# Optimization experiments

Measured on AMD Instinct MI355X. Metric: run time of the kernel, lower is better.

The kernel has to match this reference:

```python
import jax, jax.numpy as jnp
import numpy as np

B, IN, H, F, T = 4096, 1024, 1024, 128, 3
LN_EPS = 1e-5


def setup_inputs() -> dict:
    key = jax.random.key(0)
    ks = jax.random.split(key, 12)
    inp = {
        "input_": jax.random.normal(ks[0], (B, IN), jnp.float32),
        "hx": jax.random.normal(ks[1], (B, H), jnp.float32),
        "cx": jax.random.normal(ks[2], (B, H), jnp.float32),
        "topic_w": jax.random.uniform(ks[3], (B, T), jnp.float32),
        # factorized gate weights (init scales per reset_parameters)
        "w_ih_a": jax.random.normal(ks[4], (4 * H, F), jnp.float32) / jnp.sqrt(F),
        "w_ih_b": jnp.full((F, T), 0.1 / T, jnp.float32),
        "w_ih_c": jax.random.normal(ks[5], (F, IN), jnp.float32) / jnp.sqrt(IN),
        "w_hh_a": 0.1 * jax.random.normal(ks[6], (4 * H, F), jnp.float32),
        "w_hh_b": jnp.full((F, T), 0.1 / T, jnp.float32),
        "w_hh_c": 0.1 * jax.random.normal(ks[7], (F, H), jnp.float32),
        # theta transforms: weight=0, bias=1 per reset_parameters
        "th_ih_w": jnp.zeros((T, T), jnp.float32),
        "th_ih_b": jnp.ones((T,), jnp.float32),
        "th_hh_w": jnp.zeros((T, T), jnp.float32),
        "th_hh_b": jnp.ones((T,), jnp.float32),
        # layernorm params
        "ln_i_w": jnp.ones((4 * H,), jnp.float32),
        "ln_i_b": jnp.zeros((4 * H,), jnp.float32),
        "ln_h_w": jnp.ones((4 * H,), jnp.float32),
        "ln_h_b": jnp.zeros((4 * H,), jnp.float32),
        "ln_c_w": jnp.ones((H,), jnp.float32),
        "ln_c_b": jnp.zeros((H,), jnp.float32),
    }
    return inp


def _ln(x, w, b):
    mu = x.mean(-1, keepdims=True)
    var = ((x - mu) ** 2).mean(-1, keepdims=True)
    return (x - mu) * jax.lax.rsqrt(var + LN_EPS) * w + b


def reference(input_, hx, cx, topic_w,
              w_ih_a, w_ih_b, w_ih_c, w_hh_a, w_hh_b, w_hh_c,
              th_ih_w, th_ih_b, th_hh_w, th_hh_b,
              ln_i_w, ln_i_b, ln_h_w, ln_h_b, ln_c_w, ln_c_b):
    # factorized input gates: ((x @ C^T) * (theta(topic) @ B^T)) @ A^T
    scale_i = (topic_w @ th_ih_w.T + th_ih_b) @ w_ih_b.T            # [B, F]
    igates = ((input_ @ w_ih_c.T) * scale_i) @ w_ih_a.T             # [B, 4H]
    scale_h = (topic_w @ th_hh_w.T + th_hh_b) @ w_hh_b.T            # [B, F]
    hgates = ((hx @ w_hh_c.T) * scale_h) @ w_hh_a.T                 # [B, 4H]

    gates = _ln(igates, ln_i_w, ln_i_b) + _ln(hgates, ln_h_w, ln_h_b)
    i, f, g, o = jnp.split(gates, 4, axis=1)
    i = jax.nn.sigmoid(i)
    f = jax.nn.sigmoid(f)
    g = jnp.tanh(g)  # dropout p=0 -> identity
    o = jax.nn.sigmoid(o)
    cy = _ln(f * cx + i * g, ln_c_w, ln_c_b)
    hy = o * jnp.tanh(cy)
    return hy, cy
```

## Files before the change

kernel.cpp:

```cpp
#include <hip/hip_runtime.h>

typedef unsigned short ushort_t;
typedef __attribute__((ext_vector_type(8))) short bf8_t;
typedef __attribute__((ext_vector_type(4))) float f4_t;

#define B_   4096
#define IN_  1024
#define H_   1024
#define F_   128
#define G4_  4096
#define EPS_ 1e-5f

#define NG1   512
#define NPREP 256
#define NGRAM 128

__device__ __forceinline__ float us2f(unsigned short s) {
  union { unsigned int u; float f; } v;
  v.u = ((unsigned int)s) << 16;
  return v.f;
}
__device__ __forceinline__ unsigned short f2us(float f) {
  union { float f; unsigned int u; } v;
  v.f = f;
  unsigned int r = (v.u + 0x7fffu + ((v.u >> 16) & 1u)) >> 16;
  return (unsigned short)r;
}
__device__ __forceinline__ float sigf(float x) { return 1.0f / (1.0f + __expf(-x)); }
__device__ __forceinline__ float tanh_f(float x) { return 1.0f - 2.0f / (1.0f + __expf(2.0f * x)); }

__device__ __forceinline__ int detect_fp32(const void* disc) {
  return ((const unsigned int*)disc)[0] == 0x3F800000u;
}
__device__ __forceinline__ float ldf(const void* p, int i, int fp32) {
  return fp32 ? ((const float*)p)[i] : us2f(((const ushort_t*)p)[i]);
}
__device__ __forceinline__ void ld8(const void* p, int idx, float* o, int fp32) {
  if (fp32) {
    const float4* q = (const float4*)((const float*)p + idx);
    float4 v0 = q[0], v1 = q[1];
    o[0]=v0.x; o[1]=v0.y; o[2]=v0.z; o[3]=v0.w;
    o[4]=v1.x; o[5]=v1.y; o[6]=v1.z; o[7]=v1.w;
  } else {
    uint4 v = *(const uint4*)((const ushort_t*)p + idx);
    const ushort_t* pv = (const ushort_t*)&v;
    #pragma unroll
    for (int i = 0; i < 8; i++) o[i] = us2f(pv[i]);
  }
}
__device__ __forceinline__ bf8_t cvt8p(const float* f) {
  union { bf8_t v; unsigned int u[4]; } r;
  const unsigned int* ui = (const unsigned int*)f;
  #pragma unroll
  for (int i = 0; i < 4; i++) {
    unsigned int lo = ui[2 * i] + 0x8000u;
    unsigned int hi = ui[2 * i + 1] + 0x8000u;
    r.u[i] = __builtin_amdgcn_perm(hi, lo, 0x07060302u);
  }
  return r.v;
}

__global__ __launch_bounds__(256, 4) void k_stageA(
    const void* __restrict__ X0, const void* __restrict__ X1,
    const void* __restrict__ Wc0, const void* __restrict__ Wc1,
    const void* __restrict__ topic,
    const void* __restrict__ thw0, const void* __restrict__ thw1,
    const void* __restrict__ thb0, const void* __restrict__ thb1,
    const void* __restrict__ wsb0, const void* __restrict__ wsb1,
    const void* __restrict__ Ai, const void* __restrict__ Ah,
    const void* __restrict__ lnwi, const void* __restrict__ lnwh,
    ushort_t* __restrict__ wb,
    float* __restrict__ cm_i, float* __restrict__ cm_h,
    float* __restrict__ g_i, float* __restrict__ g_h,
    float* __restrict__ C0, float* __restrict__ C1)
{
  __shared__ __align__(16) char lds_raw[32768];
  int bid = blockIdx.x, tid = threadIdx.x;
  int fp32 = detect_fp32(lnwi);

  if (bid < NG1) {
    int rb = bid >> 1, mat = bid & 1;
    const void* X   = mat ? X1 : X0;
    const void* W   = mat ? Wc1 : Wc0;
    const void* thw = mat ? thw1 : thw0;
    const void* thb = mat ? thb1 : thb0;
    const void* wbp = mat ? wsb1 : wsb0;
    float* C = mat ? C1 : C0;
    int lane = tid & 63, w = tid >> 6;
    int quad = lane >> 4, lcol = lane & 15;
    int brow0 = rb * 16;

    #pragma unroll
    for (int p = 0; p < 8; p++) {
      int fl = p * 2048 + tid * 8;
      int r = fl >> 10, cidx = fl & 1023;
      float t8[8];
      ld8(X, (brow0 + r) * IN_ + cidx, t8, fp32);
      bf8_t v = cvt8p(t8);
      int byte = (r * 2048 + cidx * 2) ^ ((r & 7) << 4);
      *(bf8_t*)(lds_raw + byte) = v;
    }
    __syncthreads();

    f4_t acc[2];
    acc[0] = (f4_t){0.f, 0.f, 0.f, 0.f};
    acc[1] = (f4_t){0.f, 0.f, 0.f, 0.f};

    int wrow = w * 32 + lcol;
    int quad8 = quad * 8;
    int afbase = lcol * 2048 + quad * 16;
    int afxor = (lcol & 7) << 4;

#define AF_(kc) (*(const bf8_t*)(lds_raw + ((afbase + (kc) * 64) ^ afxor)))
#define LOADW_(buf, kc) { \
      ld8(W, (wrow)      * IN_ + (kc) * 32 + quad8, buf[0], fp32); \
      ld8(W, (wrow + 16) * IN_ + (kc) * 32 + quad8, buf[1], fp32); }
#define STEPK_(buf, kc) { \
      bf8_t af_ = AF_(kc); \
      acc[0] = __builtin_amdgcn_mfma_f32_16x16x32_bf16(af_, cvt8p(buf[0]), acc[0], 0, 0, 0); \
      acc[1] = __builtin_amdgcn_mfma_f32_16x16x32_bf16(af_, cvt8p(buf[1]), acc[1], 0, 0, 0); }

    float pb0[2][8], pb1[2][8];
    LOADW_(pb0, 0);
    LOADW_(pb1, 1);
    #pragma unroll
    for (int kc = 0; kc < 32; kc += 2) {
      STEPK_(pb0, kc);
      if (kc + 2 < 32) LOADW_(pb0, kc + 2);
      STEPK_(pb1, kc + 1);
      if (kc + 3 < 32) LOADW_(pb1, kc + 3);
    }
#undef AF_
#undef LOADW_
#undef STEPK_

    float thwf[3][3], thbf[3];
    #pragma unroll
    for (int t = 0; t < 3; t++) {
      thbf[t] = ldf(thb, t, fp32);
      #pragma unroll
      for (int t2 = 0; t2 < 3; t2++) thwf[t][t2] = ldf(thw, t * 3 + t2, fp32);
    }
    float tmpv[4][3];
    #pragma unroll
    for (int reg = 0; reg < 4; reg++) {
      int b = brow0 + quad * 4 + reg;
      float tp0 = ldf(topic, b * 3 + 0, fp32);
      float tp1 = ldf(topic, b * 3 + 1, fp32);
      float tp2 = ldf(topic, b * 3 + 2, fp32);
      #pragma unroll
      for (int t = 0; t < 3; t++)
        tmpv[reg][t] = thbf[t] + tp0 * thwf[t][0] + tp1 * thwf[t][1] + tp2 * thwf[t][2];
    }
    #pragma unroll
    for (int t = 0; t < 2; t++) {
      int f = (w * 2 + t) * 16 + lcol;
      float wv0 = ldf(wbp, f * 3 + 0, fp32);
      float wv1 = ldf(wbp, f * 3 + 1, fp32);
      float wv2 = ldf(wbp, f * 3 + 2, fp32);
      #pragma unroll
      for (int reg = 0; reg < 4; reg++) {
        float sc = tmpv[reg][0] * wv0 + tmpv[reg][1] * wv1 + tmpv[reg][2] * wv2;
        C[(brow0 + quad * 4 + reg) * F_ + f] = acc[t][reg] * sc;
      }
    }
  } else if (bid < NG1 + NPREP) {
    int t = bid - NG1;
    #pragma unroll
    for (int i = 0; i < 16; i++) {
      int e = i * 256 + tid;
      int c = e >> 9, l = (e >> 3) & 63, j = e & 7;
      int k = c * 32 + ((l >> 4) << 3) + j;
      int n = t * 16 + (l & 15);
      float v;
      if (k < 128) v = ldf(Ai, n * F_ + k, fp32) * ldf(lnwi, n, fp32);
      else         v = ldf(Ah, n * F_ + (k - 128), fp32) * ldf(lnwh, n, fp32);
      wb[(size_t)t * 4096 + e] = f2us(v);
    }
    const void* A = (tid < 128) ? Ai : Ah;
    float* cm = (tid < 128) ? cm_i : cm_h;
    int f = tid & 127;
    float s = 0.f;
    #pragma unroll
    for (int i = 0; i < 16; i++) s += ldf(A, (t * 16 + i) * F_ + f, fp32);
    atomicAdd(&cm[f], s);
  } else {
    int g = bid - (NG1 + NPREP);
    int fblk = g & 3, mat = (g >> 2) & 1, z = g >> 3;
    const void* A = mat ? Ah : Ai;
    float* G = mat ? g_h : g_i;
    float (*As)[128] = (float(*)[128])lds_raw;
    int f1_0 = fblk * 32;
    int tf2 = tid & 31, tf1 = tid >> 5;
    float acc[4][4] = {};
    int nbase = z * 256;
    for (int n0 = nbase; n0 < nbase + 256; n0 += 32) {
      #pragma unroll
      for (int j = 0; j < 2; j++) {
        int idx = tid + 256 * j;
        int nn = idx >> 4, f8 = (idx & 15) * 8;
        float t[8];
        ld8(A, (n0 + nn) * F_ + f8, t, fp32);
        #pragma unroll
        for (int i = 0; i < 8; i++) As[nn][f8 + i] = t[i];
      }
      __syncthreads();
      #pragma unroll 4
      for (int nn = 0; nn < 32; nn++) {
        float4 a1 = *(const float4*)&As[nn][f1_0 + 4 * tf1];
        float4 a2 = *(const float4*)&As[nn][4 * tf2];
        const float* x1 = (const float*)&a1;
        const float* x2 = (const float*)&a2;
        #pragma unroll
        for (int i = 0; i < 4; i++)
          #pragma unroll
          for (int j = 0; j < 4; j++) acc[i][j] += x1[i] * x2[j];
      }
      __syncthreads();
    }
    #pragma unroll
    for (int i = 0; i < 4; i++)
      #pragma unroll
      for (int j = 0; j < 4; j++)
        atomicAdd(&G[(f1_0 + 4 * tf1 + i) * F_ + 4 * tf2 + j], acc[i][j]);
  }
}

__global__ __launch_bounds__(256, 4) void k_stats2(
    const float* __restrict__ C0, const float* __restrict__ C1,
    const float* __restrict__ g_i, const float* __restrict__ g_h,
    const float* __restrict__ cm_i, const float* __restrict__ cm_h,
    float* __restrict__ mrs_i, float* __restrict__ mrs_h,
    ushort_t* __restrict__ xb)
{
  int bid = blockIdx.x;
  int rb = bid >> 1, mat = bid & 1;
  const float* C  = mat ? C1 : C0;
  const float* G  = mat ? g_h : g_i;
  const float* cm = mat ? cm_h : cm_i;
  float* mrs = mat ? mrs_h : mrs_i;
  int kbase = mat ? 128 : 0;

  int tid = threadIdx.x;
  int lane = tid & 63, w = tid >> 6;
  int quad = lane >> 4, lcol = lane & 15;
  int b0 = rb * 16;

  __shared__ float p1part[4][16];
  __shared__ float p2s[16];
  __shared__ float rs_s[16];

  bf8_t af[4];
  float p2p = 0.f;
  #pragma unroll
  for (int kc = 0; kc < 4; kc++) {
    int kb = kc * 32 + quad * 8;
    const float4* q = (const float4*)(C + (b0 + lcol) * F_ + kb);
    float4 v0 = q[0], v1 = q[1];
    float a[8] = {v0.x, v0.y, v0.z, v0.w, v1.x, v1.y, v1.z, v1.w};
    af[kc] = cvt8p(a);
    if (w == 0) {
      #pragma unroll
      for (int j = 0; j < 8; j++) p2p += a[j] * cm[kb + j];
    }
  }

  float p1p[4] = {0.f, 0.f, 0.f, 0.f};
  #pragma unroll
  for (int t = 0; t < 2; t++) {
    int colf = (w * 2 + t) * 16 + lcol;
    f4_t acc = {0.f, 0.f, 0.f, 0.f};
    #pragma unroll
    for (int kc = 0; kc < 4; kc++) {
      const float4* qg = (const float4*)(G + colf * F_ + kc * 32 + quad * 8);
      float4 w0 = qg[0], w1 = qg[1];
      float bt[8] = {w0.x, w0.y, w0.z, w0.w, w1.x, w1.y, w1.z, w1.w};
      acc = __builtin_amdgcn_mfma_f32_16x16x32_bf16(af[kc], cvt8p(bt), acc, 0, 0, 0);
    }
    #pragma unroll
    for (int reg = 0; reg < 4; reg++)
      p1p[reg] += acc[reg] * C[(b0 + quad * 4 + reg) * F_ + colf];
  }
  #pragma unroll
  for (int d = 1; d < 16; d <<= 1)
    #pragma unroll
    for (int reg = 0; reg < 4; reg++)
      p1p[reg] += __shfl_xor(p1p[reg], d, 64);
  if (lcol == 0) {
    #pragma unroll
    for (int reg = 0; reg < 4; reg++)
      p1part[w][quad * 4 + reg] = p1p[reg];
  }
  if (w == 0) {
    p2p += __shfl_xor(p2p, 16, 64);
    p2p += __shfl_xor(p2p, 32, 64);
    if (quad == 0) p2s[lcol] = p2p;
  }
  __syncthreads();
  if (tid < 16) {
    float p1 = p1part[0][tid] + p1part[1][tid] + p1part[2][tid] + p1part[3][tid];
    float E2 = p1 * (1.0f / 4096.0f);
    float mu = p2s[tid] * (1.0f / 4096.0f);
    float var = E2 - mu * mu;
    float rs = rsqrtf(var + EPS_);
    rs_s[tid] = rs;
    mrs[b0 + tid] = mu * rs;
  }
  __syncthreads();
  int f = tid & 127, half = tid >> 7;
  ushort_t* xbb = xb + (size_t)rb * 4096;
  int k = kbase + f;
  int c = k >> 5, lq = (k >> 3) & 3, j = k & 7;
  #pragma unroll
  for (int i = 0; i < 8; i++) {
    int r2 = half * 8 + i;
    int lfrag = r2 | (lq << 4);
    xbb[c * 512 + lfrag * 8 + j] = f2us(C[(b0 + r2) * F_ + f] * rs_s[r2]);
  }
}

__global__ __launch_bounds__(1024) void k_fused(
    const ushort_t* __restrict__ xb, const ushort_t* __restrict__ wb,
    const float* __restrict__ mrs_i, const float* __restrict__ mrs_h,
    const void* __restrict__ lniw, const void* __restrict__ lnib,
    const void* __restrict__ lnhw, const void* __restrict__ lnhb,
    const void* __restrict__ lncw, const void* __restrict__ lncb,
    const void* __restrict__ cx, float* __restrict__ out)
{
  __shared__ float buf[16][1028];
  __shared__ float obuf[16][1028];
  __shared__ ushort_t xs[4096];
  __shared__ float wpart[16][16][2];
  __shared__ float mu_s[16], rs_s[16];
  int tid = threadIdx.x;
  int lane = tid & 63, w = tid >> 6;
  int quad = lane >> 4, lcol = lane & 15;
  int b0 = blockIdx.x * 16;
  int fp32 = detect_fp32(lniw);

  ((unsigned long long*)xs)[tid] =
      ((const unsigned long long*)(xb + (size_t)blockIdx.x * 4096))[tid];

  float mi[4], mh[4];
  #pragma unroll
  for (int reg = 0; reg < 4; reg++) {
    mi[reg] = mrs_i[b0 + quad * 4 + reg];
    mh[reg] = mrs_h[b0 + quad * 4 + reg];
  }
  __syncthreads();

  float s1[4] = {0.f, 0.f, 0.f, 0.f}, s2[4] = {0.f, 0.f, 0.f, 0.f};

  #pragma unroll
  for (int q = 0; q < 4; q++) {
    int cg = w * 4 + q;
    int col = cg * 16 + lcol;
    float cxv[4];
    #pragma unroll
    for (int reg = 0; reg < 4; reg++)
      cxv[reg] = ldf(cx, (size_t)(b0 + quad * 4 + reg) * H_ + col, fp32);

    f4_t accg[4];
    #pragma unroll
    for (int g = 0; g < 4; g++) accg[g] = (f4_t){0.f, 0.f, 0.f, 0.f};
    #pragma unroll
    for (int c = 0; c < 8; c++) {
      bf8_t af = *(const bf8_t*)&xs[c * 512 + lane * 8];
      #pragma unroll
      for (int g = 0; g < 4; g++) {
        bf8_t bf = *(const bf8_t*)(wb + (size_t)(g * 64 + cg) * 4096 + c * 512 + lane * 8);
        accg[g] = __builtin_amdgcn_mfma_f32_16x16x32_bf16(af, bf, accg[g], 0, 0, 0);
      }
    }
    float liw0 = ldf(lniw, 0 * H_ + col, fp32), lib0 = ldf(lnib, 0 * H_ + col, fp32);
    float lhw0 = ldf(lnhw, 0 * H_ + col, fp32), lhb0 = ldf(lnhb, 0 * H_ + col, fp32);
    float liw1 = ldf(lniw, 1 * H_ + col, fp32), lib1 = ldf(lnib, 1 * H_ + col, fp32);
    float lhw1 = ldf(lnhw, 1 * H_ + col, fp32), lhb1 = ldf(lnhb, 1 * H_ + col, fp32);
    float liw2 = ldf(lniw, 2 * H_ + col, fp32), lib2 = ldf(lnib, 2 * H_ + col, fp32);
    float lhw2 = ldf(lnhw, 2 * H_ + col, fp32), lhb2 = ldf(lnhb, 2 * H_ + col, fp32);
    float liw3 = ldf(lniw, 3 * H_ + col, fp32), lib3 = ldf(lnib, 3 * H_ + col, fp32);
    float lhw3 = ldf(lnhw, 3 * H_ + col, fp32), lhb3 = ldf(lnhb, 3 * H_ + col, fp32);
    #pragma unroll
    for (int reg = 0; reg < 4; reg++) {
      int m = quad * 4 + reg;
      float gi = accg[0][reg] + lib0 + lhb0 - mi[reg] * liw0 - mh[reg] * lhw0;
      float gf = accg[1][reg] + lib1 + lhb1 - mi[reg] * liw1 - mh[reg] * lhw1;
      float gg = accg[2][reg] + lib2 + lhb2 - mi[reg] * liw2 - mh[reg] * lhw2;
      float go = accg[3][reg] + lib3 + lhb3 - mi[reg] * liw3 - mh[reg] * lhw3;
      float iv = sigf(gi), fv = sigf(gf), gv = tanh_f(gg), ov = sigf(go);
      float cval = fv * cxv[reg] + iv * gv;
      buf[m][col] = cval;
      obuf[m][col] = ov;
      s1[reg] += cval;
      s2[reg] += cval * cval;
    }
  }

  #pragma unroll
  for (int d = 1; d < 16; d <<= 1) {
    #pragma unroll
    for (int reg = 0; reg < 4; reg++) {
      s1[reg] += __shfl_xor(s1[reg], d, 64);
      s2[reg] += __shfl_xor(s2[reg], d, 64);
    }
  }
  if (lcol == 0) {
    #pragma unroll
    for (int reg = 0; reg < 4; reg++) {
      wpart[w][quad * 4 + reg][0] = s1[reg];
      wpart[w][quad * 4 + reg][1] = s2[reg];
    }
  }
  __syncthreads();
  if (tid < 16) {
    float t1 = 0.f, t2 = 0.f;
    #pragma unroll
    for (int ww = 0; ww < 16; ww++) { t1 += wpart[ww][tid][0]; t2 += wpart[ww][tid][1]; }
    float mu = t1 * (1.0f / 1024.0f);
    float var = t2 * (1.0f / 1024.0f) - mu * mu;
    mu_s[tid] = mu;
    rs_s[tid] = rsqrtf(var + EPS_);
  }
  __syncthreads();

  #pragma unroll
  for (int q = 0; q < 4; q++) {
    int col = (w * 4 + q) * 16 + lcol;
    float lw = ldf(lncw, col, fp32), lb = ldf(lncb, col, fp32);
    #pragma unroll
    for (int reg = 0; reg < 4; reg++) {
      int m = quad * 4 + reg;
      float cyv = (buf[m][col] - mu_s[m]) * rs_s[m] * lw + lb;
      out[(size_t)B_ * H_ + (size_t)(b0 + m) * H_ + col] = cyv;
      out[(size_t)(b0 + m) * H_ + col] = obuf[m][col] * tanh_f(cyv);
    }
  }
}

extern "C" void kernel_launch(void* const* d_in, const int* in_sizes, int n_in,
                              void* d_out, int out_size, void* d_ws, size_t ws_size,
                              hipStream_t stream) {
  const void* input_  = d_in[0];
  const void* hx      = d_in[1];
  const void* cx      = d_in[2];
  const void* topic   = d_in[3];
  const void* w_ih_a  = d_in[4];
  const void* w_ih_b  = d_in[5];
  const void* w_ih_c  = d_in[6];
  const void* w_hh_a  = d_in[7];
  const void* w_hh_b  = d_in[8];
  const void* w_hh_c  = d_in[9];
  const void* th_ih_w = d_in[10];
  const void* th_ih_b = d_in[11];
  const void* th_hh_w = d_in[12];
  const void* th_hh_b = d_in[13];
  const void* ln_i_w  = d_in[14];
  const void* ln_i_b  = d_in[15];
  const void* ln_h_w  = d_in[16];
  const void* ln_h_b  = d_in[17];
  const void* ln_c_w  = d_in[18];
  const void* ln_c_b  = d_in[19];

  float* w = (float*)d_ws;
  float* c1    = w;
  float* c2    = c1 + B_ * F_;
  float* g_i   = c2 + B_ * F_;
  float* g_h   = g_i + F_ * F_;
  float* cm_i  = g_h + F_ * F_;
  float* cm_h  = cm_i + F_;
  float* mrs_i = cm_h + F_;
  float* mrs_h = mrs_i + B_;
  ushort_t* xb = (ushort_t*)(mrs_h + B_);
  ushort_t* wbf = xb + (size_t)B_ * 256;

  hipMemsetAsync(g_i, 0, (size_t)(2 * F_ * F_ + 2 * F_) * sizeof(float), stream);

  k_stageA<<<dim3(NG1 + NPREP + NGRAM), dim3(256), 0, stream>>>(
      input_, hx, w_ih_c, w_hh_c, topic,
      th_ih_w, th_hh_w, th_ih_b, th_hh_b, w_ih_b, w_hh_b,
      w_ih_a, w_hh_a, ln_i_w, ln_h_w,
      wbf, cm_i, cm_h, g_i, g_h, c1, c2);
  k_stats2<<<dim3(512), dim3(256), 0, stream>>>(
      c1, c2, g_i, g_h, cm_i, cm_h, mrs_i, mrs_h, xb);
  k_fused<<<dim3(256), dim3(1024), 0, stream>>>(
      xb, wbf, mrs_i, mrs_h,
      ln_i_w, ln_i_b, ln_h_w, ln_h_b, ln_c_w, ln_c_b, cx, (float*)d_out);
}
```

Before: 216.2 us.

## Split-K the first factor GEMM and fuse LN stats into final kernel

The input-projection GEMM is split along K into two halves per row block, accumulating into a zeroed C buffer with atomics. Launch bounds and LDS use change to allow more resident blocks. The per-row LayerNorm statistics, the topic scaling and the bf16 packing move from a separate kernel into the final fused kernel through shared memory, removing one launch and the global round trip through xb/mrs. The cost is float atomics, a larger memset, and extra shared memory in the fused kernel.

```diff
diff --git a/kernel.cpp b/kernel.cpp
--- a/kernel.cpp
+++ b/kernel.cpp
@@ -8,10 +8,9 @@
 #define IN_  1024
 #define H_   1024
 #define F_   128
-#define G4_  4096
 #define EPS_ 1e-5f
 
-#define NG1   512
+#define NG1   1024
 #define NPREP 256
 #define NGRAM 128
 
@@ -60,13 +59,9 @@
   return r.v;
 }
 
-__global__ __launch_bounds__(256, 4) void k_stageA(
+__global__ __launch_bounds__(256, 8) void k_stageA(
     const void* __restrict__ X0, const void* __restrict__ X1,
     const void* __restrict__ Wc0, const void* __restrict__ Wc1,
-    const void* __restrict__ topic,
-    const void* __restrict__ thw0, const void* __restrict__ thw1,
-    const void* __restrict__ thb0, const void* __restrict__ thb1,
-    const void* __restrict__ wsb0, const void* __restrict__ wsb1,
     const void* __restrict__ Ai, const void* __restrict__ Ah,
     const void* __restrict__ lnwi, const void* __restrict__ lnwh,
     ushort_t* __restrict__ wb,
@@ -74,30 +69,27 @@
     float* __restrict__ g_i, float* __restrict__ g_h,
     float* __restrict__ C0, float* __restrict__ C1)
 {
-  __shared__ __align__(16) char lds_raw[32768];
+  __shared__ __align__(16) char lds_raw[16384];
   int bid = blockIdx.x, tid = threadIdx.x;
   int fp32 = detect_fp32(lnwi);
 
   if (bid < NG1) {
-    int rb = bid >> 1, mat = bid & 1;
-    const void* X   = mat ? X1 : X0;
-    const void* W   = mat ? Wc1 : Wc0;
-    const void* thw = mat ? thw1 : thw0;
-    const void* thb = mat ? thb1 : thb0;
-    const void* wbp = mat ? wsb1 : wsb0;
+    int rb = bid >> 2, mat = (bid >> 1) & 1, kh = bid & 1;
+    const void* X = mat ? X1 : X0;
+    const void* W = mat ? Wc1 : Wc0;
     float* C = mat ? C1 : C0;
     int lane = tid & 63, w = tid >> 6;
     int quad = lane >> 4, lcol = lane & 15;
-    int brow0 = rb * 16;
-
-    #pragma unroll
-    for (int p = 0; p < 8; p++) {
+    int brow0 = rb * 16, k0 = kh * 512;
+
+    #pragma unroll
+    for (int p = 0; p < 4; p++) {
       int fl = p * 2048 + tid * 8;
-      int r = fl >> 10, cidx = fl & 1023;
+      int r = fl >> 9, cidx = fl & 511;
       float t8[8];
-      ld8(X, (brow0 + r) * IN_ + cidx, t8, fp32);
+      ld8(X, (brow0 + r) * IN_ + k0 + cidx, t8, fp32);
       bf8_t v = cvt8p(t8);
-      int byte = (r * 2048 + cidx * 2) ^ ((r & 7) << 4);
+      int byte = (r * 1024 + cidx * 2) ^ ((r & 7) << 4);
       *(bf8_t*)(lds_raw + byte) = v;
     }
     __syncthreads();
@@ -108,13 +100,13 @@
 
     int wrow = w * 32 + lcol;
     int quad8 = quad * 8;
-    int afbase = lcol * 2048 + quad * 16;
+    int afbase = lcol * 1024 + quad * 16;
     int afxor = (lcol & 7) << 4;
 
 #define AF_(kc) (*(const bf8_t*)(lds_raw + ((afbase + (kc) * 64) ^ afxor)))
 #define LOADW_(buf, kc) { \
-      ld8(W, (wrow)      * IN_ + (kc) * 32 + quad8, buf[0], fp32); \
-      ld8(W, (wrow + 16) * IN_ + (kc) * 32 + quad8, buf[1], fp32); }
+      ld8(W, (wrow)      * IN_ + k0 + (kc) * 32 + quad8, buf[0], fp32); \
+      ld8(W, (wrow + 16) * IN_ + k0 + (kc) * 32 + quad8, buf[1], fp32); }
 #define STEPK_(buf, kc) { \
       bf8_t af_ = AF_(kc); \
       acc[0] = __builtin_amdgcn_mfma_f32_16x16x32_bf16(af_, cvt8p(buf[0]), acc[0], 0, 0, 0); \
@@ -124,45 +116,22 @@
     LOADW_(pb0, 0);
     LOADW_(pb1, 1);
     #pragma unroll
-    for (int kc = 0; kc < 32; kc += 2) {
+    for (int kc = 0; kc < 16; kc += 2) {
       STEPK_(pb0, kc);
-      if (kc + 2 < 32) LOADW_(pb0, kc + 2);
+      if (kc + 2 < 16) LOADW_(pb0, kc + 2);
       STEPK_(pb1, kc + 1);
-      if (kc + 3 < 32) LOADW_(pb1, kc + 3);
+      if (kc + 3 < 16) LOADW_(pb1, kc + 3);
     }
 #undef AF_
 #undef LOADW_
 #undef STEPK_
 
-    float thwf[3][3], thbf[3];
-    #pragma unroll
-    for (int t = 0; t < 3; t++) {
-      thbf[t] = ldf(thb, t, fp32);
-      #pragma unroll
-      for (int t2 = 0; t2 < 3; t2++) thwf[t][t2] = ldf(thw, t * 3 + t2, fp32);
-    }
-    float tmpv[4][3];
-    #pragma unroll
-    for (int reg = 0; reg < 4; reg++) {
-      int b = brow0 + quad * 4 + reg;
-      float tp0 = ldf(topic, b * 3 + 0, fp32);
-      float tp1 = ldf(topic, b * 3 + 1, fp32);
-      float tp2 = ldf(topic, b * 3 + 2, fp32);
-      #pragma unroll
-      for (int t = 0; t < 3; t++)
-        tmpv[reg][t] = thbf[t] + tp0 * thwf[t][0] + tp1 * thwf[t][1] + tp2 * thwf[t][2];
-    }
     #pragma unroll
     for (int t = 0; t < 2; t++) {
       int f = (w * 2 + t) * 16 + lcol;
-      float wv0 = ldf(wbp, f * 3 + 0, fp32);
-      float wv1 = ldf(wbp, f * 3 + 1, fp32);
-      float wv2 = ldf(wbp, f * 3 + 2, fp32);
-      #pragma unroll
-      for (int reg = 0; reg < 4; reg++) {
-        float sc = tmpv[reg][0] * wv0 + tmpv[reg][1] * wv1 + tmpv[reg][2] * wv2;
-        C[(brow0 + quad * 4 + reg) * F_ + f] = acc[t][reg] * sc;
-      }
+      #pragma unroll
+      for (int reg = 0; reg < 4; reg++)
+        atomicAdd(&C[(brow0 + quad * 4 + reg) * F_ + f], acc[t][reg]);
     }
   } else if (bid < NG1 + NPREP) {
     int t = bid - NG1;
@@ -226,128 +195,147 @@
   }
 }
 
-__global__ __launch_bounds__(256, 4) void k_stats2(
-    const float* __restrict__ C0, const float* __restrict__ C1,
+__global__ __launch_bounds__(1024) void k_fused2(
+    const float* __restrict__ C0g, const float* __restrict__ C1g,
     const float* __restrict__ g_i, const float* __restrict__ g_h,
     const float* __restrict__ cm_i, const float* __restrict__ cm_h,
-    float* __restrict__ mrs_i, float* __restrict__ mrs_h,
-    ushort_t* __restrict__ xb)
-{
-  int bid = blockIdx.x;
-  int rb = bid >> 1, mat = bid & 1;
-  const float* C  = mat ? C1 : C0;
-  const float* G  = mat ? g_h : g_i;
-  const float* cm = mat ? cm_h : cm_i;
-  float* mrs = mat ? mrs_h : mrs_i;
-  int kbase = mat ? 128 : 0;
-
-  int tid = threadIdx.x;
-  int lane = tid & 63, w = tid >> 6;
-  int quad = lane >> 4, lcol = lane & 15;
-  int b0 = rb * 16;
-
-  __shared__ float p1part[4][16];
-  __shared__ float p2s[16];
-  __shared__ float rs_s[16];
-
-  bf8_t af[4];
-  float p2p = 0.f;
-  #pragma unroll
-  for (int kc = 0; kc < 4; kc++) {
-    int kb = kc * 32 + quad * 8;
-    const float4* q = (const float4*)(C + (b0 + lcol) * F_ + kb);
-    float4 v0 = q[0], v1 = q[1];
-    float a[8] = {v0.x, v0.y, v0.z, v0.w, v1.x, v1.y, v1.z, v1.w};
-    af[kc] = cvt8p(a);
-    if (w == 0) {
-      #pragma unroll
-      for (int j = 0; j < 8; j++) p2p += a[j] * cm[kb + j];
-    }
-  }
-
-  float p1p[4] = {0.f, 0.f, 0.f, 0.f};
-  #pragma unroll
-  for (int t = 0; t < 2; t++) {
-    int colf = (w * 2 + t) * 16 + lcol;
-    f4_t acc = {0.f, 0.f, 0.f, 0.f};
-    #pragma unroll
-    for (int kc = 0; kc < 4; kc++) {
-      const float4* qg = (const float4*)(G + colf * F_ + kc * 32 + quad * 8);
-      float4 w0 = qg[0], w1 = qg[1];
-      float bt[8] = {w0.x, w0.y, w0.z, w0.w, w1.x, w1.y, w1.z, w1.w};
-      acc = __builtin_amdgcn_mfma_f32_16x16x32_bf16(af[kc], cvt8p(bt), acc, 0, 0, 0);
-    }
-    #pragma unroll
-    for (int reg = 0; reg < 4; reg++)
-      p1p[reg] += acc[reg] * C[(b0 + quad * 4 + reg) * F_ + colf];
-  }
-  #pragma unroll
-  for (int d = 1; d < 16; d <<= 1)
-    #pragma unroll
-    for (int reg = 0; reg < 4; reg++)
-      p1p[reg] += __shfl_xor(p1p[reg], d, 64);
-  if (lcol == 0) {
-    #pragma unroll
-    for (int reg = 0; reg < 4; reg++)
-      p1part[w][quad * 4 + reg] = p1p[reg];
-  }
-  if (w == 0) {
-    p2p += __shfl_xor(p2p, 16, 64);
-    p2p += __shfl_xor(p2p, 32, 64);
-    if (quad == 0) p2s[lcol] = p2p;
-  }
-  __syncthreads();
-  if (tid < 16) {
-    float p1 = p1part[0][tid] + p1part[1][tid] + p1part[2][tid] + p1part[3][tid];
-    float E2 = p1 * (1.0f / 4096.0f);
-    float mu = p2s[tid] * (1.0f / 4096.0f);
-    float var = E2 - mu * mu;
-    float rs = rsqrtf(var + EPS_);
-    rs_s[tid] = rs;
-    mrs[b0 + tid] = mu * rs;
-  }
-  __syncthreads();
-  int f = tid & 127, half = tid >> 7;
-  ushort_t* xbb = xb + (size_t)rb * 4096;
-  int k = kbase + f;
-  int c = k >> 5, lq = (k >> 3) & 3, j = k & 7;
-  #pragma unroll
-  for (int i = 0; i < 8; i++) {
-    int r2 = half * 8 + i;
-    int lfrag = r2 | (lq << 4);
-    xbb[c * 512 + lfrag * 8 + j] = f2us(C[(b0 + r2) * F_ + f] * rs_s[r2]);
-  }
-}
-
-__global__ __launch_bounds__(1024) void k_fused(
-    const ushort_t* __restrict__ xb, const ushort_t* __restrict__ wb,
-    const float* __restrict__ mrs_i, const float* __restrict__ mrs_h,
+    const void* __restrict__ topic,
+    const void* __restrict__ thw0, const void* __restrict__ thw1,
+    const void* __restrict__ thb0, const void* __restrict__ thb1,
+    const void* __restrict__ wsb0, const void* __restrict__ wsb1,
+    const ushort_t* __restrict__ wb,
     const void* __restrict__ lniw, const void* __restrict__ lnib,
     const void* __restrict__ lnhw, const void* __restrict__ lnhb,
     const void* __restrict__ lncw, const void* __restrict__ lncb,
     const void* __restrict__ cx, float* __restrict__ out)
 {
+  __shared__ float Cs[2][16][132];
+  __shared__ __align__(16) ushort_t xs[4096];
   __shared__ float buf[16][1028];
   __shared__ float obuf[16][1028];
-  __shared__ ushort_t xs[4096];
+  __shared__ float p1part[2][4][16];
+  __shared__ float p2s[2][16];
+  __shared__ float rs2_s[2][16];
+  __shared__ float mrs_s[2][16];
   __shared__ float wpart[16][16][2];
   __shared__ float mu_s[16], rs_s[16];
+
   int tid = threadIdx.x;
   int lane = tid & 63, w = tid >> 6;
   int quad = lane >> 4, lcol = lane & 15;
   int b0 = blockIdx.x * 16;
   int fp32 = detect_fp32(lniw);
 
-  ((unsigned long long*)xs)[tid] =
-      ((const unsigned long long*)(xb + (size_t)blockIdx.x * 4096))[tid];
+  {
+    int mat = tid >> 9, rem = tid & 511;
+    int row = rem >> 5, f0 = (rem & 31) * 4;
+    const float* C = mat ? C1g : C0g;
+    const void* thw = mat ? thw1 : thw0;
+    const void* thb = mat ? thb1 : thb0;
+    const void* wbp = mat ? wsb1 : wsb0;
+    float tp0 = ldf(topic, (b0 + row) * 3 + 0, fp32);
+    float tp1 = ldf(topic, (b0 + row) * 3 + 1, fp32);
+    float tp2 = ldf(topic, (b0 + row) * 3 + 2, fp32);
+    float tv[3];
+    #pragma unroll
+    for (int t = 0; t < 3; t++)
+      tv[t] = ldf(thb, t, fp32) + tp0 * ldf(thw, t * 3 + 0, fp32)
+            + tp1 * ldf(thw, t * 3 + 1, fp32) + tp2 * ldf(thw, t * 3 + 2, fp32);
+    float4 v = *(const float4*)&C[(size_t)(b0 + row) * F_ + f0];
+    const float* vp = (const float*)&v;
+    #pragma unroll
+    for (int j = 0; j < 4; j++) {
+      int f = f0 + j;
+      float sc = tv[0] * ldf(wbp, f * 3 + 0, fp32)
+               + tv[1] * ldf(wbp, f * 3 + 1, fp32)
+               + tv[2] * ldf(wbp, f * 3 + 2, fp32);
+      Cs[mat][row][f] = vp[j] * sc;
+    }
+  }
+  __syncthreads();
+
+  if (w < 8) {
+    int w2 = w & 3, smat = w >> 2;
+    const float* G  = smat ? g_h : g_i;
+    const float* cm = smat ? cm_h : cm_i;
+    bf8_t af[4];
+    float p2p = 0.f;
+    #pragma unroll
+    for (int kc = 0; kc < 4; kc++) {
+      int kb = kc * 32 + quad * 8;
+      float a[8];
+      #pragma unroll
+      for (int j = 0; j < 8; j++) a[j] = Cs[smat][lcol][kb + j];
+      af[kc] = cvt8p(a);
+      if (w2 == 0) {
+        #pragma unroll
+        for (int j = 0; j < 8; j++) p2p += a[j] * cm[kb + j];
+      }
+    }
+    float p1p[4] = {0.f, 0.f, 0.f, 0.f};
+    #pragma unroll
+    for (int t = 0; t < 2; t++) {
+      int colf = (w2 * 2 + t) * 16 + lcol;
+      f4_t acc = {0.f, 0.f, 0.f, 0.f};
+      #pragma unroll
+      for (int kc = 0; kc < 4; kc++) {
+        const float4* qg = (const float4*)(G + colf * F_ + kc * 32 + quad * 8);
+        float4 w0 = qg[0], w1 = qg[1];
+        float bt[8] = {w0.x, w0.y, w0.z, w0.w, w1.x, w1.y, w1.z, w1.w};
+        acc = __builtin_amdgcn_mfma_f32_16x16x32_bf16(af[kc], cvt8p(bt), acc, 0, 0, 0);
+      }
+      #pragma unroll
+      for (int reg = 0; reg < 4; reg++)
+        p1p[reg] += acc[reg] * Cs[smat][quad * 4 + reg][colf];
+    }
+    #pragma unroll
+    for (int d = 1; d < 16; d <<= 1)
+      #pragma unroll
+      for (int reg = 0; reg < 4; reg++)
+        p1p[reg] += __shfl_xor(p1p[reg], d, 64);
+    if (lcol == 0) {
+      #pragma unroll
+      for (int reg = 0; reg < 4; reg++)
+        p1part[smat][w2][quad * 4 + reg] = p1p[reg];
+    }
+    if (w2 == 0) {
+      p2p += __shfl_xor(p2p, 16, 64);
+      p2p += __shfl_xor(p2p, 32, 64);
+      if (quad == 0) p2s[smat][lcol] = p2p;
+    }
+  }
+  __syncthreads();
+  if (tid < 32) {
+    int m = tid >> 4, r = tid & 15;
+    float p1 = p1part[m][0][r] + p1part[m][1][r] + p1part[m][2][r] + p1part[m][3][r];
+    float E2 = p1 * (1.0f / 4096.0f);
+    float mu = p2s[m][r] * (1.0f / 4096.0f);
+    float rs = rsqrtf(E2 - mu * mu + EPS_);
+    rs2_s[m][r] = rs;
+    mrs_s[m][r] = mu * rs;
+  }
+  __syncthreads();
+
+  if (tid < 512) {
+    int m = tid >> 8, tt = tid & 255;
+    int f = tt & 127, half = tt >> 7;
+    int k = m * 128 + f;
+    int c = k >> 5, lq = (k >> 3) & 3, j = k & 7;
+    #pragma unroll
+    for (int i = 0; i < 8; i++) {
+      int r2 = half * 8 + i;
+      int lfrag = r2 | (lq << 4);
+      xs[c * 512 + lfrag * 8 + j] = f2us(Cs[m][r2][f] * rs2_s[m][r2]);
+    }
+  }
+  __syncthreads();
 
   float mi[4], mh[4];
   #pragma unroll
   for (int reg = 0; reg < 4; reg++) {
-    mi[reg] = mrs_i[b0 + quad * 4 + reg];
-    mh[reg] = mrs_h[b0 + quad * 4 + reg];
-  }
-  __syncthreads();
+    mi[reg] = mrs_s[0][quad * 4 + reg];
+    mh[reg] = mrs_s[1][quad * 4 + reg];
+  }
 
   float s1[4] = {0.f, 0.f, 0.f, 0.f}, s2[4] = {0.f, 0.f, 0.f, 0.f};
 
@@ -468,21 +456,16 @@
   float* g_h   = g_i + F_ * F_;
   float* cm_i  = g_h + F_ * F_;
   float* cm_h  = cm_i + F_;
-  float* mrs_i = cm_h + F_;
-  float* mrs_h = mrs_i + B_;
-  ushort_t* xb = (ushort_t*)(mrs_h + B_);
-  ushort_t* wbf = xb + (size_t)B_ * 256;
-
-  hipMemsetAsync(g_i, 0, (size_t)(2 * F_ * F_ + 2 * F_) * sizeof(float), stream);
+  ushort_t* wbf = (ushort_t*)(cm_h + F_);
+
+  hipMemsetAsync(c1, 0, (size_t)(2 * B_ * F_ + 2 * F_ * F_ + 2 * F_) * sizeof(float), stream);
 
   k_stageA<<<dim3(NG1 + NPREP + NGRAM), dim3(256), 0, stream>>>(
-      input_, hx, w_ih_c, w_hh_c, topic,
-      th_ih_w, th_hh_w, th_ih_b, th_hh_b, w_ih_b, w_hh_b,
+      input_, hx, w_ih_c, w_hh_c,
       w_ih_a, w_hh_a, ln_i_w, ln_h_w,
       wbf, cm_i, cm_h, g_i, g_h, c1, c2);
-  k_stats2<<<dim3(512), dim3(256), 0, stream>>>(
-      c1, c2, g_i, g_h, cm_i, cm_h, mrs_i, mrs_h, xb);
-  k_fused<<<dim3(256), dim3(1024), 0, stream>>>(
-      xb, wbf, mrs_i, mrs_h,
-      ln_i_w, ln_i_b, ln_h_w, ln_h_b, ln_c_w, ln_c_b, cx, (float*)d_out);
-}
+  k_fused2<<<dim3(256), dim3(1024), 0, stream>>>(
+      c1, c2, g_i, g_h, cm_i, cm_h,
+      topic, th_ih_w, th_hh_w, th_ih_b, th_hh_b, w_ih_b, w_hh_b,
+      wbf, ln_i_w, ln_i_b, ln_h_w, ln_h_b, ln_c_w, ln_c_b, cx, (float*)d_out);
+}
```

New measurement: 218.4 us. About the same (+1.0%).
